# Kernel tuning notes

Hardware: AMD Instinct MI355X
Metric: run time of the kernel (lower is better)

The kernel has to match this reference:

```python
import jax, jax.numpy as jnp
import numpy as np

N_NODES = 50000
N_EDGES = 400000
F_IN = 70
E_DIM = 4
HID = 128
HEADS = 4


def _add_self_loops(src, dst, edge_attr, n):
    # PyG GATConv(add_self_loops=True, fill_value='mean' when edge_dim is set):
    # self-loop edge_attr = per-dst-node mean of incoming edge_attr.
    cnt = jax.ops.segment_sum(jnp.ones((src.shape[0],), edge_attr.dtype), dst, n)
    loop_attr = jax.ops.segment_sum(edge_attr, dst, n) / jnp.clip(cnt, 1.0)[:, None]
    loop = jnp.arange(n, dtype=src.dtype)
    return (jnp.concatenate([src, loop]), jnp.concatenate([dst, loop]),
            jnp.concatenate([edge_attr, loop_attr], axis=0))


def _gat_layer(x, src, dst, e_attr, W, a_src, a_dst, We, a_edge, b, concat):
    # W: [in, H*D]; a_src/a_dst/a_edge: [H, D]; We: [edge_dim, H*D]
    n = x.shape[0]
    H, D = a_src.shape
    xs = (x @ W).reshape(n, H, D)                      # [N,H,D]
    s_src = jnp.einsum('nhd,hd->nh', xs, a_src)        # [N,H]
    s_dst = jnp.einsum('nhd,hd->nh', xs, a_dst)
    ee = (e_attr @ We).reshape(-1, H, D)               # [E,H,D]
    s_edge = jnp.einsum('ehd,hd->eh', ee, a_edge)
    alpha = jax.nn.leaky_relu(s_src[src] + s_dst[dst] + s_edge, 0.2)  # [E,H]
    # segment softmax over edges grouped by destination node
    m = jax.ops.segment_max(alpha, dst, n)
    m = jnp.where(jnp.isfinite(m), m, 0.0)
    ex = jnp.exp(alpha - m[dst])
    denom = jax.ops.segment_sum(ex, dst, n)
    alpha = ex / (denom[dst] + 1e-16)
    msg = xs[src] * alpha[..., None]                   # [E,H,D] -- dominant traffic
    agg = jax.ops.segment_sum(msg, dst, n)             # [N,H,D]
    out = agg.reshape(n, H * D) if concat else agg.mean(axis=1)
    return out + b


def _layer_norm(x, g, b, eps=1e-5):
    mu = x.mean(-1, keepdims=True)
    var = ((x - mu) ** 2).mean(-1, keepdims=True)
    return (x - mu) * jax.lax.rsqrt(var + eps) * g + b


def setup_inputs() -> dict:
    key = jax.random.key(0)
    ks = jax.random.split(key, 24)
    f32 = jnp.float32
    node_features = jax.random.normal(ks[0], (N_NODES, F_IN), f32)
    edge_index = jax.random.randint(ks[1], (2, N_EDGES), 0, N_NODES, jnp.int32)
    edge_attr = jax.random.uniform(ks[2], (N_EDGES, E_DIM), f32)
    s = 0.1
    return {
        'node_features': node_features,
        'edge_index': edge_index,
        'edge_attr': edge_attr,
        'W1': jax.random.normal(ks[3], (F_IN, HEADS * HID), f32) * s,
        'as1': jax.random.normal(ks[4], (HEADS, HID), f32) * s,
        'ad1': jax.random.normal(ks[5], (HEADS, HID), f32) * s,
        'We1': jax.random.normal(ks[6], (E_DIM, HEADS * HID), f32) * s,
        'ae1': jax.random.normal(ks[7], (HEADS, HID), f32) * s,
        'b1': jnp.zeros((HEADS * HID,), f32),
        # GAT layer 2: 512 -> 128, 1 head, mean
        'W2': jax.random.normal(ks[8], (HEADS * HID, HID), f32) * s,
        'as2': jax.random.normal(ks[9], (1, HID), f32) * s,
        'ad2': jax.random.normal(ks[10], (1, HID), f32) * s,
        'We2': jax.random.normal(ks[11], (E_DIM, HID), f32) * s,
        'ae2': jax.random.normal(ks[12], (1, HID), f32) * s,
        'b2': jnp.zeros((HID,), f32),
        'ln_g': jnp.ones((HID,), f32),
        'ln_b': jnp.zeros((HID,), f32),
        'pw': jax.random.normal(ks[13], (HID, 8), f32) * s,
        'pb': jnp.zeros((8,), f32),
        'dw': jax.random.normal(ks[14], (HID, 4), f32) * s,
        'db': jnp.zeros((4,), f32),
    }


def reference(node_features, edge_index, edge_attr, W1, as1, ad1, We1, ae1, b1,
              W2, as2, ad2, We2, ae2, b2, ln_g, ln_b, pw, pb, dw, db):
    n = node_features.shape[0]
    src, dst, ea = _add_self_loops(edge_index[0], edge_index[1], edge_attr, n)
    x = jax.nn.gelu(_gat_layer(node_features, src, dst, ea, W1, as1, ad1, We1, ae1, b1, True), approximate=False)
    x = jax.nn.gelu(_gat_layer(x, src, dst, ea, W2, as2, ad2, We2, ae2, b2, False), approximate=False)
    x = _layer_norm(x, ln_g, ln_b)
    return (x @ pw + pb, x @ dw + db)
```

## Files before the change

kernel.cpp:

```cpp
#include <hip/hip_runtime.h>
#include <hip/hip_bf16.h>
#include <math.h>

#define NN 50000
#define NE 400000
#define FIN 70
#define EDIM 4
#define HIDD 128
#define NHEAD 4
constexpr int ET = NE + NN;
constexpr int KP1 = 96;
constexpr int NFP = 72;
constexpr int SCB = (NN + 255) / 256;

constexpr size_t al4(size_t x){ return (x + 3) & ~size_t(3); }
constexpr size_t CNT_O   = 0;
constexpr size_t ZEND    = al4(CNT_O + NN);
constexpr size_t CSR_O   = ZEND;
constexpr size_t BSUM_O  = al4(CSR_O + NN + 1);
constexpr size_t BOFF_O  = al4(BSUM_O + 256);
constexpr size_t EPK_O   = al4(BOFF_O + 256);
constexpr size_t EXF1_O  = al4(EPK_O + (size_t)ET*4);
constexpr size_t EXF2_O  = al4(EXF1_O + (size_t)ET*4);
constexpr size_t SS1_O   = al4(EXF2_O + ET);
constexpr size_t SD1_O   = al4(SS1_O + (size_t)NN*4);
constexpr size_t SS2_O   = al4(SD1_O + (size_t)NN*4);
constexpr size_t SD2_O   = al4(SS2_O + NN);
constexpr size_t CST_O   = al4(SD2_O + NN);
constexpr size_t W1T_O   = al4(CST_O + 2048);
constexpr size_t W2T_O   = al4(W1T_O + 4*128*KP1/2);
constexpr size_t NFB_O   = al4(W2T_O + 128*512/2);
constexpr size_t AGG_O   = al4(NFB_O + (size_t)NN*NFP/2);
constexpr size_t X1_O    = al4(AGG_O + (size_t)4*NN*KP1/2);
constexpr size_t XS2_O   = al4(X1_O + (size_t)NN*512/2);

constexpr int VS1 = 0;
constexpr int VD1 = 320;
constexpr int VE1 = 640;
constexpr int VE2 = 656;
constexpr int VS2 = 704;
constexpr int VD2 = 1216;

typedef short s8v __attribute__((ext_vector_type(8)));
typedef float f4v __attribute__((ext_vector_type(4)));

__device__ __forceinline__ float gelu_exact(float x){
  return 0.5f * x * (1.f + erff(x * 0.70710678118654752440f));
}
__device__ __forceinline__ unsigned short f2b(float v){
  __hip_bfloat16 b = __float2bfloat16(v);
  return *(unsigned short*)&b;
}
__device__ __forceinline__ float b2f(unsigned u_lo16){
  return __uint_as_float(u_lo16 << 16);
}
__device__ __forceinline__ unsigned pk2(float lo, float hi){
  return (unsigned)f2b(lo) | ((unsigned)f2b(hi) << 16);
}
__device__ __forceinline__ float lrelu(float x){ return x > 0.f ? x : 0.2f * x; }

__global__ void k_deg(const int* __restrict__ ei, int* __restrict__ cnt){
  int e = blockIdx.x * 256 + threadIdx.x;
  if (e >= NE) return;
  atomicAdd(&cnt[ei[NE + e]], 1);
}

__global__ void k_scan1(const int* __restrict__ cnt, int* __restrict__ bsum){
  __shared__ int ws[4];
  int t = threadIdx.x, lane = t & 63, w = t >> 6;
  int i = blockIdx.x * 256 + t;
  int v = (i < NN) ? cnt[i] + 1 : 0;
  for (int o = 32; o; o >>= 1) v += __shfl_down(v, o);
  if (lane == 0) ws[w] = v;
  __syncthreads();
  if (t == 0) bsum[blockIdx.x] = ws[0] + ws[1] + ws[2] + ws[3];
}

__global__ void k_scan2(const int* __restrict__ bsum, int* __restrict__ boff){
  __shared__ int ws[4];
  int t = threadIdx.x, lane = t & 63, w = t >> 6;
  int v = (t < SCB) ? bsum[t] : 0;
  int x = v;
  #pragma unroll
  for (int o = 1; o < 64; o <<= 1){ int u = __shfl_up(x, o); if (lane >= o) x += u; }
  if (lane == 63) ws[w] = x;
  __syncthreads();
  if (w == 0 && lane < 4){
    int y = ws[lane];
    #pragma unroll
    for (int o = 1; o < 4; o <<= 1){ int u = __shfl_up(y, o); if (lane >= o) y += u; }
    ws[lane] = y;
  }
  __syncthreads();
  int incl = x + (w > 0 ? ws[w - 1] : 0);
  if (t < SCB) boff[t] = incl - v;
}

__global__ void k_scan3(const int* __restrict__ cnt, const int* __restrict__ boff,
                        int* __restrict__ csr){
  __shared__ int ws[4];
  int t = threadIdx.x, lane = t & 63, w = t >> 6;
  int i = blockIdx.x * 256 + t;
  int v = (i < NN) ? cnt[i] + 1 : 0;
  int x = v;
  #pragma unroll
  for (int o = 1; o < 64; o <<= 1){ int u = __shfl_up(x, o); if (lane >= o) x += u; }
  if (lane == 63) ws[w] = x;
  __syncthreads();
  if (w == 0 && lane < 4){
    int y = ws[lane];
    #pragma unroll
    for (int o = 1; o < 4; o <<= 1){ int u = __shfl_up(y, o); if (lane >= o) y += u; }
    ws[lane] = y;
  }
  __syncthreads();
  if (i < NN) csr[i + 1] = boff[blockIdx.x] + (w > 0 ? ws[w - 1] : 0) + x;
  if (i == 0) csr[0] = 0;
}

__global__ void k_fill(const int* __restrict__ ei, const float* __restrict__ ea,
                       const int* __restrict__ csr, int* __restrict__ cnt,
                       int4* __restrict__ epk, const float* __restrict__ ss1,
                       const float* __restrict__ sd1, const float* __restrict__ C,
                       float4* __restrict__ exf){
  int e = blockIdx.x * 256 + threadIdx.x;
  if (e >= NE) return;
  int s = ei[e], d = ei[NE + e];
  int r = atomicSub(&cnt[d], 1);
  int p = csr[d] + r - 1;
  float4 a = *(const float4*)&ea[(size_t)e * 4];
  epk[p] = make_int4(s, d, (int)pk2(a.x, a.y), (int)pk2(a.z, a.w));
  float4 ssv = *(const float4*)&ss1[(size_t)s * 4];
  float4 sdv = *(const float4*)&sd1[(size_t)d * 4];
  float e0 = __expf(lrelu(ssv.x + sdv.x + a.x*C[VE1+0] + a.y*C[VE1+4] + a.z*C[VE1+8]  + a.w*C[VE1+12]));
  float e1 = __expf(lrelu(ssv.y + sdv.y + a.x*C[VE1+1] + a.y*C[VE1+5] + a.z*C[VE1+9]  + a.w*C[VE1+13]));
  float e2 = __expf(lrelu(ssv.z + sdv.z + a.x*C[VE1+2] + a.y*C[VE1+6] + a.z*C[VE1+10] + a.w*C[VE1+14]));
  float e3 = __expf(lrelu(ssv.w + sdv.w + a.x*C[VE1+3] + a.y*C[VE1+7] + a.z*C[VE1+11] + a.w*C[VE1+15]));
  exf[p] = make_float4(e0, e1, e2, e3);
}

__global__ void k_loopself(const int* __restrict__ csr, int4* __restrict__ epk,
                           const float* __restrict__ ss1, const float* __restrict__ sd1,
                           const float* __restrict__ C, float4* __restrict__ exf){
  int n = blockIdx.x * 256 + threadIdx.x;
  if (n >= NN) return;
  int a = csr[n], b = csr[n + 1];
  int deg = b - a - 1;
  float s0 = 0.f, s1 = 0.f, s2 = 0.f, s3 = 0.f;
  for (int p = a; p < b - 1; ++p){
    int4 v = epk[p];
    s0 += b2f((unsigned)v.z & 0xffffu); s1 += b2f((unsigned)v.z >> 16);
    s2 += b2f((unsigned)v.w & 0xffffu); s3 += b2f((unsigned)v.w >> 16);
  }
  float inv = 1.f / (float)(deg > 1 ? deg : 1);
  float m0 = s0*inv, m1 = s1*inv, m2 = s2*inv, m3 = s3*inv;
  epk[b - 1] = make_int4(n, n, (int)pk2(m0, m1), (int)pk2(m2, m3));
  float4 ssv = *(const float4*)&ss1[(size_t)n * 4];
  float4 sdv = *(const float4*)&sd1[(size_t)n * 4];
  float e0 = __expf(lrelu(ssv.x + sdv.x + m0*C[VE1+0] + m1*C[VE1+4] + m2*C[VE1+8]  + m3*C[VE1+12]));
  float e1 = __expf(lrelu(ssv.y + sdv.y + m0*C[VE1+1] + m1*C[VE1+5] + m2*C[VE1+9]  + m3*C[VE1+13]));
  float e2 = __expf(lrelu(ssv.z + sdv.z + m0*C[VE1+2] + m1*C[VE1+6] + m2*C[VE1+10] + m3*C[VE1+14]));
  float e3 = __expf(lrelu(ssv.w + sdv.w + m0*C[VE1+3] + m1*C[VE1+7] + m2*C[VE1+11] + m3*C[VE1+15]));
  exf[b - 1] = make_float4(e0, e1, e2, e3);
}

__global__ void k_prep(const float* __restrict__ W1, const float* __restrict__ as1,
                       const float* __restrict__ ad1, const float* __restrict__ We1,
                       const float* __restrict__ ae1, const float* __restrict__ W2,
                       const float* __restrict__ as2, const float* __restrict__ ad2,
                       const float* __restrict__ We2, const float* __restrict__ ae2,
                       float* __restrict__ C){
  int t = threadIdx.x;
  if (t < 280){
    int k = t >> 2, h = t & 3;
    float s = 0.f, d = 0.f;
    for (int dd = 0; dd < 128; ++dd){
      float w = W1[k*512 + h*128 + dd];
      s += w * as1[h*128 + dd];
      d += w * ad1[h*128 + dd];
    }
    C[VS1 + t] = s; C[VD1 + t] = d;
  }
  if (t < 16){
    int k = t >> 2, h = t & 3;
    float s = 0.f;
    for (int dd = 0; dd < 128; ++dd) s += We1[k*512 + h*128 + dd] * ae1[h*128 + dd];
    C[VE1 + t] = s;
  }
  if (t < 4){
    float s = 0.f;
    for (int dd = 0; dd < 128; ++dd) s += We2[t*128 + dd] * ae2[dd];
    C[VE2 + t] = s;
  }
  {
    float s = 0.f, d = 0.f;
    for (int dd = 0; dd < 128; ++dd){
      float w = W2[t*128 + dd];
      s += w * as2[dd];
      d += w * ad2[dd];
    }
    C[VS2 + t] = s; C[VD2 + t] = d;
  }
}

__global__ void k_tw(const float* __restrict__ W1, const float* __restrict__ W2,
                     unsigned short* __restrict__ W1t, unsigned short* __restrict__ W2t){
  int i = blockIdx.x * 256 + threadIdx.x;
  if (i < 4*128*KP1){
    int k = i % KP1, n = (i / KP1) & 127, h = i / (KP1*128);
    float v = (k < FIN) ? W1[k*512 + h*128 + n] : 0.f;
    W1t[i] = f2b(v);
  } else {
    int j = i - 4*128*KP1;
    if (j < 128*512){
      int k = j & 511, n = j >> 9;
      W2t[j] = f2b(W2[k*128 + n]);
    }
  }
}

__global__ __launch_bounds__(256) void k_cnfs1(const float* __restrict__ nf,
    const float* __restrict__ C, unsigned short* __restrict__ nfb,
    float* __restrict__ ss1, float* __restrict__ sd1){
  int lane = threadIdx.x & 63, w = threadIdx.x >> 6;
  int n = blockIdx.x * 4 + w;
  if (n >= NN) return;
  int c0 = lane * 2;
  bool act = lane < 35;
  float v0 = 0.f, v1 = 0.f;
  if (act){
    v0 = nf[(size_t)n * FIN + c0];
    v1 = nf[(size_t)n * FIN + c0 + 1];
  }
  if (lane < 36) *(unsigned*)&nfb[(size_t)n * NFP + c0] = act ? pk2(v0, v1) : 0u;
  float sh[4] = {0,0,0,0}, dh[4] = {0,0,0,0};
  if (act){
    float4 cs0 = *(const float4*)&C[VS1 + c0*4];
    float4 cs1 = *(const float4*)&C[VS1 + (c0+1)*4];
    float4 cd0 = *(const float4*)&C[VD1 + c0*4];
    float4 cd1 = *(const float4*)&C[VD1 + (c0+1)*4];
    sh[0] = v0*cs0.x + v1*cs1.x; sh[1] = v0*cs0.y + v1*cs1.y;
    sh[2] = v0*cs0.z + v1*cs1.z; sh[3] = v0*cs0.w + v1*cs1.w;
    dh[0] = v0*cd0.x + v1*cd1.x; dh[1] = v0*cd0.y + v1*cd1.y;
    dh[2] = v0*cd0.z + v1*cd1.z; dh[3] = v0*cd0.w + v1*cd1.w;
  }
  #pragma unroll
  for (int o = 32; o; o >>= 1){
    #pragma unroll
    for (int h = 0; h < 4; ++h){
      sh[h] += __shfl_xor(sh[h], o);
      dh[h] += __shfl_xor(dh[h], o);
    }
  }
  if (lane == 0){
    *(float4*)&ss1[(size_t)n*4] = make_float4(sh[0], sh[1], sh[2], sh[3]);
    *(float4*)&sd1[(size_t)n*4] = make_float4(dh[0], dh[1], dh[2], dh[3]);
  }
}

__global__ void k_al2(const int4* __restrict__ epk, const float* __restrict__ ss2,
                      const float* __restrict__ sd2, const float* __restrict__ C,
                      float* __restrict__ ex2){
  int p = blockIdx.x * 256 + threadIdx.x;
  if (p >= ET) return;
  int4 pk = epk[p];
  int s = pk.x, d = pk.y;
  float ax = b2f((unsigned)pk.z & 0xffffu), ay = b2f((unsigned)pk.z >> 16);
  float az = b2f((unsigned)pk.w & 0xffffu), aw = b2f((unsigned)pk.w >> 16);
  ex2[p] = __expf(lrelu(ss2[s] + sd2[d] +
             ax*C[VE2] + ay*C[VE2+1] + az*C[VE2+2] + aw*C[VE2+3]));
}

template<int MODE>
__global__ __launch_bounds__(256) void k_mfma(
    const unsigned short* __restrict__ A, int lda, long aSz,
    const unsigned short* __restrict__ Bt, long bSz,
    void* __restrict__ Cout, const float* __restrict__ bias,
    int M, int KP){
  int z = blockIdx.y;
  A  += (size_t)z * aSz;
  Bt += (size_t)z * bSz;
  __shared__ unsigned short sm[10240];
  unsigned short* As = sm;
  unsigned short* Bs = sm + 5120;
  int tid = threadIdx.x, lane = tid & 63, w = tid >> 6;
  int wm = w & 1, wn = w >> 1;
  int row0 = blockIdx.x * 128;
  f4v acc[4][4] = {};
  int r4 = tid >> 2, c4 = tid & 3;
  for (int k0 = 0; k0 < KP; k0 += 32){
    #pragma unroll
    for (int half = 0; half < 2; ++half){
      int r = r4 + half * 64;
      int gr = row0 + r;
      uint4 va = make_uint4(0,0,0,0);
      if (gr < M) va = *(const uint4*)&A[(size_t)gr * lda + k0 + c4*8];
      *(uint4*)&As[r*40 + c4*8] = va;
      uint4 vb = *(const uint4*)&Bt[(size_t)r * lda + k0 + c4*8];
      *(uint4*)&Bs[r*40 + c4*8] = vb;
    }
    __syncthreads();
    s8v af[4], bf[4];
    #pragma unroll
    for (int i = 0; i < 4; ++i){
      af[i] = *(const s8v*)&As[(wm*64 + i*16 + (lane & 15))*40 + (lane >> 4)*8];
      bf[i] = *(const s8v*)&Bs[(wn*64 + i*16 + (lane & 15))*40 + (lane >> 4)*8];
    }
    #pragma unroll
    for (int mi = 0; mi < 4; ++mi)
      #pragma unroll
      for (int ni = 0; ni < 4; ++ni)
        acc[mi][ni] = __builtin_amdgcn_mfma_f32_16x16x32_bf16(af[mi], bf[ni], acc[mi][ni], 0, 0, 0);
    __syncthreads();
  }
  int cq = lane & 15, rq = lane >> 4;
  float bv[4];
  if (MODE == 1){
    #pragma unroll
    for (int ni = 0; ni < 4; ++ni) bv[ni] = bias[z*128 + wn*64 + ni*16 + cq];
  }
  #pragma unroll
  for (int pass = 0; pass < 2; ++pass){
    if (wm == pass){
      #pragma unroll
      for (int mi = 0; mi < 4; ++mi)
        #pragma unroll
        for (int r = 0; r < 4; ++r){
          int lr = mi*16 + rq*4 + r;
          #pragma unroll
          for (int ni = 0; ni < 4; ++ni){
            float v = acc[mi][ni][r];
            if (MODE == 1) v = gelu_exact(v + bv[ni]);
            sm[lr*136 + wn*64 + ni*16 + cq] = f2b(v);
          }
        }
    }
    __syncthreads();
    #pragma unroll
    for (int j = 0; j < 4; ++j){
      int cid = tid + j*256;
      int lr = cid >> 4, ch = cid & 15;
      int grow = row0 + pass*64 + lr;
      if (grow < M){
        uint4 v = *(const uint4*)&sm[lr*136 + ch*8];
        if (MODE == 1)
          *(uint4*)&((unsigned short*)Cout)[(size_t)grow*512 + z*128 + ch*8] = v;
        else
          *(uint4*)&((unsigned short*)Cout)[(size_t)grow*128 + ch*8] = v;
      }
    }
    __syncthreads();
  }
}

__global__ __launch_bounds__(256) void k_aggnf(const int* __restrict__ csr,
    const int4* __restrict__ epk, const float4* __restrict__ exf,
    const unsigned short* __restrict__ nfb, unsigned short* __restrict__ agg){
  int lane = threadIdx.x & 63, w = threadIdx.x >> 6;
  int n = blockIdx.x * 4 + w;
  if (n >= NN) return;
  int off = __builtin_amdgcn_readfirstlane(csr[n]);
  int end = __builtin_amdgcn_readfirstlane(csr[n + 1]);
  int col = lane * 2;
  bool act = lane < 36;
  float d0=0,d1=0,d2=0,d3=0;
  float a00=0,a01=0,a10=0,a11=0,a20=0,a21=0,a30=0,a31=0;
  int p = off;
  for (; p + 2 <= end; p += 2){
    int s0 = epk[p].x, s1 = epk[p+1].x;
    float4 e0 = exf[p], e1 = exf[p+1];
    unsigned u0 = 0, u1 = 0;
    if (act){
      u0 = *(const unsigned*)&nfb[(size_t)s0 * NFP + col];
      u1 = *(const unsigned*)&nfb[(size_t)s1 * NFP + col];
    }
    d0 += e0.x + e1.x; d1 += e0.y + e1.y; d2 += e0.z + e1.z; d3 += e0.w + e1.w;
    float v00 = b2f(u0 & 0xffffu), v01 = b2f(u0 >> 16);
    float v10 = b2f(u1 & 0xffffu), v11 = b2f(u1 >> 16);
    a00 += e0.x*v00 + e1.x*v10; a01 += e0.x*v01 + e1.x*v11;
    a10 += e0.y*v00 + e1.y*v10; a11 += e0.y*v01 + e1.y*v11;
    a20 += e0.z*v00 + e1.z*v10; a21 += e0.z*v01 + e1.z*v11;
    a30 += e0.w*v00 + e1.w*v10; a31 += e0.w*v01 + e1.w*v11;
  }
  if (p < end){
    int s0 = epk[p].x;
    float4 e0 = exf[p];
    unsigned u0 = 0;
    if (act) u0 = *(const unsigned*)&nfb[(size_t)s0 * NFP + col];
    d0 += e0.x; d1 += e0.y; d2 += e0.z; d3 += e0.w;
    float v00 = b2f(u0 & 0xffffu), v01 = b2f(u0 >> 16);
    a00 += e0.x*v00; a01 += e0.x*v01;
    a10 += e0.y*v00; a11 += e0.y*v01;
    a20 += e0.z*v00; a21 += e0.z*v01;
    a30 += e0.w*v00; a31 += e0.w*v01;
  }
  float i0 = 1.f/(d0+1e-16f), i1 = 1.f/(d1+1e-16f);
  float i2 = 1.f/(d2+1e-16f), i3 = 1.f/(d3+1e-16f);
  constexpr size_t HS = (size_t)NN * KP1;
  size_t base = (size_t)n * KP1 + col;
  if (act){
    *(unsigned*)&agg[base]        = pk2(a00*i0, a01*i0);
    *(unsigned*)&agg[base +   HS] = pk2(a10*i1, a11*i1);
    *(unsigned*)&agg[base + 2*HS] = pk2(a20*i2, a21*i2);
    *(unsigned*)&agg[base + 3*HS] = pk2(a30*i3, a31*i3);
  } else if (lane < 48){
    *(unsigned*)&agg[base]        = 0u;
    *(unsigned*)&agg[base +   HS] = 0u;
    *(unsigned*)&agg[base + 2*HS] = 0u;
    *(unsigned*)&agg[base + 3*HS] = 0u;
  }
}

__global__ void k_s2(const unsigned short* __restrict__ x1, const float* __restrict__ C,
                     float* __restrict__ ss2, float* __restrict__ sd2){
  int tid = threadIdx.x, lane = tid & 63;
  int n = blockIdx.x * 4 + (tid >> 6);
  if (n >= NN) return;
  uint4 xv = *(const uint4*)&x1[(size_t)n * 512 + lane * 8];
  float xf[8];
  xf[0] = b2f(xv.x & 0xffffu); xf[1] = b2f(xv.x >> 16);
  xf[2] = b2f(xv.y & 0xffffu); xf[3] = b2f(xv.y >> 16);
  xf[4] = b2f(xv.z & 0xffffu); xf[5] = b2f(xv.z >> 16);
  xf[6] = b2f(xv.w & 0xffffu); xf[7] = b2f(xv.w >> 16);
  float s = 0.f, d = 0.f;
  #pragma unroll
  for (int j = 0; j < 8; ++j){
    s += xf[j] * C[VS2 + lane*8 + j];
    d += xf[j] * C[VD2 + lane*8 + j];
  }
  for (int o = 32; o; o >>= 1){ s += __shfl_down(s, o); d += __shfl_down(d, o); }
  if (lane == 0){ ss2[n] = s; sd2[n] = d; }
}

__global__ __launch_bounds__(256) void k_agg2(
    const int* __restrict__ csr, const int4* __restrict__ epk,
    const float* __restrict__ ex2, const unsigned short* __restrict__ xs2b,
    const float* __restrict__ b2, const float* __restrict__ lng,
    const float* __restrict__ lnb, const float* __restrict__ pw,
    const float* __restrict__ pb, const float* __restrict__ dwm,
    const float* __restrict__ dbv, float* __restrict__ out){
  int lane = threadIdx.x & 63, w = threadIdx.x >> 6;
  int n = blockIdx.x * 4 + w;
  if (n >= NN) return;
  int off = __builtin_amdgcn_readfirstlane(csr[n]);
  int end = __builtin_amdgcn_readfirstlane(csr[n + 1]);
  int c0 = lane * 2;
  float acc0 = 0.f, acc1 = 0.f, den = 0.f;
  int p = off;
  for (; p + 4 <= end; p += 4){
    int s0 = epk[p].x, s1 = epk[p+1].x, s2 = epk[p+2].x, s3 = epk[p+3].x;
    float e0 = ex2[p], e1 = ex2[p+1], e2 = ex2[p+2], e3 = ex2[p+3];
    unsigned u0 = *(const unsigned*)&xs2b[(size_t)s0 * 128 + c0];
    unsigned u1 = *(const unsigned*)&xs2b[(size_t)s1 * 128 + c0];
    unsigned u2 = *(const unsigned*)&xs2b[(size_t)s2 * 128 + c0];
    unsigned u3 = *(const unsigned*)&xs2b[(size_t)s3 * 128 + c0];
    den += (e0 + e1) + (e2 + e3);
    acc0 += e0*b2f(u0 & 0xffffu) + e1*b2f(u1 & 0xffffu)
          + e2*b2f(u2 & 0xffffu) + e3*b2f(u3 & 0xffffu);
    acc1 += e0*b2f(u0 >> 16) + e1*b2f(u1 >> 16)
          + e2*b2f(u2 >> 16) + e3*b2f(u3 >> 16);
  }
  for (; p + 2 <= end; p += 2){
    int s0 = epk[p].x, s1 = epk[p+1].x;
    float e0 = ex2[p], e1 = ex2[p+1];
    unsigned u0 = *(const unsigned*)&xs2b[(size_t)s0 * 128 + c0];
    unsigned u1 = *(const unsigned*)&xs2b[(size_t)s1 * 128 + c0];
    den += e0 + e1;
    acc0 += e0*b2f(u0 & 0xffffu) + e1*b2f(u1 & 0xffffu);
    acc1 += e0*b2f(u0 >> 16) + e1*b2f(u1 >> 16);
  }
  if (p < end){
    int s0 = epk[p].x;
    float e0 = ex2[p];
    unsigned u0 = *(const unsigned*)&xs2b[(size_t)s0 * 128 + c0];
    den += e0;
    acc0 += e0*b2f(u0 & 0xffffu);
    acc1 += e0*b2f(u0 >> 16);
  }
  float invd = 1.f / (den + 1e-16f);
  float g0 = gelu_exact(acc0 * invd + b2[c0]);
  float g1 = gelu_exact(acc1 * invd + b2[c0 + 1]);
  float s = g0 + g1;
  #pragma unroll
  for (int o = 32; o; o >>= 1) s += __shfl_xor(s, o);
  float mu = s * (1.f / 128.f);
  float e0 = g0 - mu, e1 = g1 - mu;
  float q = e0*e0 + e1*e1;
  #pragma unroll
  for (int o = 32; o; o >>= 1) q += __shfl_xor(q, o);
  float rstd = rsqrtf(q * (1.f / 128.f) + 1e-5f);
  float y0 = e0 * rstd * lng[c0] + lnb[c0];
  float y1 = e1 * rstd * lng[c0 + 1] + lnb[c0 + 1];
  float pr[12];
  #pragma unroll
  for (int j = 0; j < 8; ++j) pr[j] = y0 * pw[c0*8 + j] + y1 * pw[(c0+1)*8 + j];
  #pragma unroll
  for (int j = 0; j < 4; ++j) pr[8+j] = y0 * dwm[c0*4 + j] + y1 * dwm[(c0+1)*4 + j];
  #pragma unroll
  for (int o = 32; o; o >>= 1)
    #pragma unroll
    for (int j = 0; j < 12; ++j) pr[j] += __shfl_xor(pr[j], o);
  if (lane == 0){
    #pragma unroll
    for (int j = 0; j < 8; ++j) out[(size_t)n*8 + j] = pr[j] + pb[j];
    #pragma unroll
    for (int j = 0; j < 4; ++j) out[(size_t)NN*8 + (size_t)n*4 + j] = pr[8+j] + dbv[j];
  }
}

extern "C" void kernel_launch(void* const* d_in, const int* in_sizes, int n_in,
                              void* d_out, int out_size, void* d_ws, size_t ws_size,
                              hipStream_t stream){
  const float* nf  = (const float*)d_in[0];
  const int*   ei  = (const int*)  d_in[1];
  const float* ea  = (const float*)d_in[2];
  const float* W1  = (const float*)d_in[3];
  const float* as1 = (const float*)d_in[4];
  const float* ad1 = (const float*)d_in[5];
  const float* We1 = (const float*)d_in[6];
  const float* ae1 = (const float*)d_in[7];
  const float* b1  = (const float*)d_in[8];
  const float* W2  = (const float*)d_in[9];
  const float* as2 = (const float*)d_in[10];
  const float* ad2 = (const float*)d_in[11];
  const float* We2 = (const float*)d_in[12];
  const float* ae2 = (const float*)d_in[13];
  const float* b2  = (const float*)d_in[14];
  const float* lng = (const float*)d_in[15];
  const float* lnb = (const float*)d_in[16];
  const float* pw  = (const float*)d_in[17];
  const float* pb  = (const float*)d_in[18];
  const float* dw  = (const float*)d_in[19];
  const float* db  = (const float*)d_in[20];
  float* out = (float*)d_out;

  float* wf = (float*)d_ws;
  int*      cnt  = (int*)     (wf + CNT_O);
  int*      csr  = (int*)     (wf + CSR_O);
  int*      bsum = (int*)     (wf + BSUM_O);
  int*      boff = (int*)     (wf + BOFF_O);
  int4*     epk  = (int4*)    (wf + EPK_O);
  float4*   exf1 = (float4*)  (wf + EXF1_O);
  float*    ex2  =            (wf + EXF2_O);
  float*    ss1  =            (wf + SS1_O);
  float*    sd1  =            (wf + SD1_O);
  float*    ss2  =            (wf + SS2_O);
  float*    sd2  =            (wf + SD2_O);
  float*    Cc   =            (wf + CST_O);
  unsigned short* W1t = (unsigned short*)(wf + W1T_O);
  unsigned short* W2t = (unsigned short*)(wf + W2T_O);
  unsigned short* nfb = (unsigned short*)(wf + NFB_O);
  unsigned short* agg = (unsigned short*)(wf + AGG_O);
  unsigned short* x1  = (unsigned short*)(wf + X1_O);
  unsigned short* xs2b= (unsigned short*)(wf + XS2_O);

  hipMemsetAsync(cnt, 0, NN * sizeof(int), stream);
  k_prep<<<1, 512, 0, stream>>>(W1, as1, ad1, We1, ae1, W2, as2, ad2, We2, ae2, Cc);
  k_tw<<<(4*128*KP1 + 128*512 + 255) / 256, 256, 0, stream>>>(W1, W2, W1t, W2t);
  k_cnfs1<<<(NN + 3) / 4, 256, 0, stream>>>(nf, Cc, nfb, ss1, sd1);
  k_deg<<<(NE + 255) / 256, 256, 0, stream>>>(ei, cnt);
  k_scan1<<<SCB, 256, 0, stream>>>(cnt, bsum);
  k_scan2<<<1, 256, 0, stream>>>(bsum, boff);
  k_scan3<<<SCB, 256, 0, stream>>>(cnt, boff, csr);
  k_fill<<<(NE + 255) / 256, 256, 0, stream>>>(ei, ea, csr, cnt, epk, ss1, sd1, Cc, exf1);
  k_loopself<<<(NN + 255) / 256, 256, 0, stream>>>(csr, epk, ss1, sd1, Cc, exf1);
  k_aggnf<<<(NN + 3) / 4, 256, 0, stream>>>(csr, epk, exf1, nfb, agg);
  k_mfma<1><<<dim3((NN + 127) / 128, 4), 256, 0, stream>>>(
      agg, KP1, (long)NN * KP1, W1t, (long)128 * KP1, x1, b1, NN, KP1);
  k_s2<<<(NN + 3) / 4, 256, 0, stream>>>(x1, Cc, ss2, sd2);
  k_mfma<2><<<dim3((NN + 127) / 128, 1), 256, 0, stream>>>(
      x1, 512, 0, W2t, 0, xs2b, nullptr, NN, 512);
  k_al2<<<(ET + 255) / 256, 256, 0, stream>>>(epk, ss2, sd2, Cc, ex2);
  k_agg2<<<(NN + 3) / 4, 256, 0, stream>>>(csr, epk, ex2, xs2b,
                                           b2, lng, lnb, pw, pb, dw, db, out);
}
```

Baseline: 387.4 us.

## Use direct-to-LDS swizzled loads in MFMA GEMM, fuse layer-2 score dots, fast GELU

The MFMA GEMM now loads A and B tiles with global_load_lds into an XOR-swizzled, unpadded LDS layout. The MFMA operands are swapped so each lane can write four bf16 results straight to global memory, which drops the LDS-staged epilogue and its barriers. The separate k_s2 kernel is removed: the per-node attention dot products for layer 2 are computed inside the layer-2 GEMM from the A tiles already sitting in LDS. Exact erf-based GELU is replaced with an Abramowitz-Stegun polynomial approximation, which adds a small numerical error in exchange for cheaper math.

```diff
diff --git a/kernel.cpp b/kernel.cpp
--- a/kernel.cpp
+++ b/kernel.cpp
@@ -44,9 +44,6 @@
 typedef short s8v __attribute__((ext_vector_type(8)));
 typedef float f4v __attribute__((ext_vector_type(4)));
 
-__device__ __forceinline__ float gelu_exact(float x){
-  return 0.5f * x * (1.f + erff(x * 0.70710678118654752440f));
-}
 __device__ __forceinline__ unsigned short f2b(float v){
   __hip_bfloat16 b = __float2bfloat16(v);
   return *(unsigned short*)&b;
@@ -58,6 +55,23 @@
   return (unsigned)f2b(lo) | ((unsigned)f2b(hi) << 16);
 }
 __device__ __forceinline__ float lrelu(float x){ return x > 0.f ? x : 0.2f * x; }
+
+__device__ __forceinline__ float gelu_fast(float x){
+  float z = x * 0.70710678118654752440f;
+  float a = fabsf(z);
+  float t = 1.f / (1.f + 0.3275911f * a);
+  float p = ((((1.061405429f*t - 1.453152027f)*t + 1.421413741f)*t
+              - 0.284496736f)*t + 0.254829592f)*t;
+  float erfv = 1.f - p * __expf(-a * a);
+  erfv = copysignf(erfv, z);
+  return 0.5f * x * (1.f + erfv);
+}
+
+__device__ __forceinline__ void gl16(const unsigned short* g, unsigned short* l){
+  __builtin_amdgcn_global_load_lds(
+      (const __attribute__((address_space(1))) unsigned int*)g,
+      (__attribute__((address_space(3))) unsigned int*)l, 16, 0, 0);
+}
 
 __global__ void k_deg(const int* __restrict__ ei, int* __restrict__ cnt){
   int e = blockIdx.x * 256 + threadIdx.x;
@@ -275,81 +289,91 @@
 __global__ __launch_bounds__(256) void k_mfma(
     const unsigned short* __restrict__ A, int lda, long aSz,
     const unsigned short* __restrict__ Bt, long bSz,
-    void* __restrict__ Cout, const float* __restrict__ bias,
+    unsigned short* __restrict__ Cout, const float* __restrict__ bias,
+    const float* __restrict__ Cv, float* __restrict__ ss2, float* __restrict__ sd2,
     int M, int KP){
   int z = blockIdx.y;
   A  += (size_t)z * aSz;
   Bt += (size_t)z * bSz;
-  __shared__ unsigned short sm[10240];
-  unsigned short* As = sm;
-  unsigned short* Bs = sm + 5120;
+  __shared__ unsigned short As[128 * 32];
+  __shared__ unsigned short Bs[128 * 32];
   int tid = threadIdx.x, lane = tid & 63, w = tid >> 6;
   int wm = w & 1, wn = w >> 1;
   int row0 = blockIdx.x * 128;
   f4v acc[4][4] = {};
-  int r4 = tid >> 2, c4 = tid & 3;
+  int rl = lane >> 2, cslot = lane & 3;
+  int m15 = lane & 15, j = lane >> 4;
+  float s2a = 0.f, s2d = 0.f;
+  int sr = tid >> 1, shf = tid & 1;
+  int ssw = (sr ^ (sr >> 2)) & 3;
   for (int k0 = 0; k0 < KP; k0 += 32){
     #pragma unroll
     for (int half = 0; half < 2; ++half){
-      int r = r4 + half * 64;
-      int gr = row0 + r;
-      uint4 va = make_uint4(0,0,0,0);
-      if (gr < M) va = *(const uint4*)&A[(size_t)gr * lda + k0 + c4*8];
-      *(uint4*)&As[r*40 + c4*8] = va;
-      uint4 vb = *(const uint4*)&Bt[(size_t)r * lda + k0 + c4*8];
-      *(uint4*)&Bs[r*40 + c4*8] = vb;
+      int rb = w * 16 + half * 64;
+      int r = rb + rl;
+      int cs = cslot ^ ((r ^ (r >> 2)) & 3);
+      int gr = row0 + r; if (gr >= M) gr = M - 1;
+      gl16(A + (size_t)gr * lda + k0 + cs * 8, &As[rb * 32]);
+      gl16(Bt + (size_t)r * lda + k0 + cs * 8, &Bs[rb * 32]);
     }
     __syncthreads();
     s8v af[4], bf[4];
     #pragma unroll
-    for (int i = 0; i < 4; ++i){
-      af[i] = *(const s8v*)&As[(wm*64 + i*16 + (lane & 15))*40 + (lane >> 4)*8];
-      bf[i] = *(const s8v*)&Bs[(wn*64 + i*16 + (lane & 15))*40 + (lane >> 4)*8];
+    for (int t = 0; t < 4; ++t){
+      int ra = wm*64 + t*16 + m15;
+      af[t] = *(const s8v*)&As[ra*32 + ((j ^ ((ra ^ (ra >> 2)) & 3)) * 8)];
+      int rb2 = wn*64 + t*16 + m15;
+      bf[t] = *(const s8v*)&Bs[rb2*32 + ((j ^ ((rb2 ^ (rb2 >> 2)) & 3)) * 8)];
+    }
+    if (MODE == 2){
+      #pragma unroll
+      for (int cc = 0; cc < 2; ++cc){
+        int c = shf * 2 + cc;
+        int kb = k0 + ((c ^ ssw) * 8);
+        s8v xv = *(const s8v*)&As[sr*32 + c*8];
+        #pragma unroll
+        for (int t2 = 0; t2 < 8; ++t2){
+          float xf = b2f((unsigned short)xv[t2]);
+          s2a += xf * Cv[VS2 + kb + t2];
+          s2d += xf * Cv[VD2 + kb + t2];
+        }
+      }
     }
     #pragma unroll
     for (int mi = 0; mi < 4; ++mi)
       #pragma unroll
       for (int ni = 0; ni < 4; ++ni)
-        acc[mi][ni] = __builtin_amdgcn_mfma_f32_16x16x32_bf16(af[mi], bf[ni], acc[mi][ni], 0, 0, 0);
+        acc[mi][ni] = __builtin_amdgcn_mfma_f32_16x16x32_bf16(bf[ni], af[mi], acc[mi][ni], 0, 0, 0);
     __syncthreads();
   }
   int cq = lane & 15, rq = lane >> 4;
-  float bv[4];
-  if (MODE == 1){
-    #pragma unroll
-    for (int ni = 0; ni < 4; ++ni) bv[ni] = bias[z*128 + wn*64 + ni*16 + cq];
-  }
-  #pragma unroll
-  for (int pass = 0; pass < 2; ++pass){
-    if (wm == pass){
+  #pragma unroll
+  for (int mi = 0; mi < 4; ++mi){
+    int grow = row0 + wm*64 + mi*16 + cq;
+    if (grow < M){
       #pragma unroll
-      for (int mi = 0; mi < 4; ++mi)
-        #pragma unroll
-        for (int r = 0; r < 4; ++r){
-          int lr = mi*16 + rq*4 + r;
-          #pragma unroll
-          for (int ni = 0; ni < 4; ++ni){
-            float v = acc[mi][ni][r];
-            if (MODE == 1) v = gelu_exact(v + bv[ni]);
-            sm[lr*136 + wn*64 + ni*16 + cq] = f2b(v);
-          }
+      for (int ni = 0; ni < 4; ++ni){
+        int gc = wn*64 + ni*16 + rq*4;
+        float v0 = acc[mi][ni][0], v1 = acc[mi][ni][1];
+        float v2 = acc[mi][ni][2], v3 = acc[mi][ni][3];
+        if (MODE == 1){
+          float4 bv = *(const float4*)&bias[z*128 + gc];
+          v0 = gelu_fast(v0 + bv.x); v1 = gelu_fast(v1 + bv.y);
+          v2 = gelu_fast(v2 + bv.z); v3 = gelu_fast(v3 + bv.w);
+          *(uint2*)&Cout[(size_t)grow*512 + z*128 + gc] = make_uint2(pk2(v0,v1), pk2(v2,v3));
+        } else {
+          *(uint2*)&Cout[(size_t)grow*128 + gc] = make_uint2(pk2(v0,v1), pk2(v2,v3));
         }
-    }
-    __syncthreads();
-    #pragma unroll
-    for (int j = 0; j < 4; ++j){
-      int cid = tid + j*256;
-      int lr = cid >> 4, ch = cid & 15;
-      int grow = row0 + pass*64 + lr;
-      if (grow < M){
-        uint4 v = *(const uint4*)&sm[lr*136 + ch*8];
-        if (MODE == 1)
-          *(uint4*)&((unsigned short*)Cout)[(size_t)grow*512 + z*128 + ch*8] = v;
-        else
-          *(uint4*)&((unsigned short*)Cout)[(size_t)grow*128 + ch*8] = v;
       }
     }
-    __syncthreads();
+  }
+  if (MODE == 2){
+    float oa = s2a + __shfl_xor(s2a, 1);
+    float od = s2d + __shfl_xor(s2d, 1);
+    if (shf == 0){
+      int grow = row0 + sr;
+      if (grow < M){ ss2[grow] = oa; sd2[grow] = od; }
+    }
   }
 }
 
@@ -409,27 +433,6 @@
     *(unsigned*)&agg[base + 2*HS] = 0u;
     *(unsigned*)&agg[base + 3*HS] = 0u;
   }
-}
-
-__global__ void k_s2(const unsigned short* __restrict__ x1, const float* __restrict__ C,
-                     float* __restrict__ ss2, float* __restrict__ sd2){
-  int tid = threadIdx.x, lane = tid & 63;
-  int n = blockIdx.x * 4 + (tid >> 6);
-  if (n >= NN) return;
-  uint4 xv = *(const uint4*)&x1[(size_t)n * 512 + lane * 8];
-  float xf[8];
-  xf[0] = b2f(xv.x & 0xffffu); xf[1] = b2f(xv.x >> 16);
-  xf[2] = b2f(xv.y & 0xffffu); xf[3] = b2f(xv.y >> 16);
-  xf[4] = b2f(xv.z & 0xffffu); xf[5] = b2f(xv.z >> 16);
-  xf[6] = b2f(xv.w & 0xffffu); xf[7] = b2f(xv.w >> 16);
-  float s = 0.f, d = 0.f;
-  #pragma unroll
-  for (int j = 0; j < 8; ++j){
-    s += xf[j] * C[VS2 + lane*8 + j];
-    d += xf[j] * C[VD2 + lane*8 + j];
-  }
-  for (int o = 32; o; o >>= 1){ s += __shfl_down(s, o); d += __shfl_down(d, o); }
-  if (lane == 0){ ss2[n] = s; sd2[n] = d; }
 }
 
 __global__ __launch_bounds__(256) void k_agg2(
@@ -478,8 +481,8 @@
     acc1 += e0*b2f(u0 >> 16);
   }
   float invd = 1.f / (den + 1e-16f);
-  float g0 = gelu_exact(acc0 * invd + b2[c0]);
-  float g1 = gelu_exact(acc1 * invd + b2[c0 + 1]);
+  float g0 = gelu_fast(acc0 * invd + b2[c0]);
+  float g1 = gelu_fast(acc1 * invd + b2[c0 + 1]);
   float s = g0 + g1;
   #pragma unroll
   for (int o = 32; o; o >>= 1) s += __shfl_xor(s, o);
@@ -493,18 +496,18 @@
   float y1 = e1 * rstd * lng[c0 + 1] + lnb[c0 + 1];
   float pr[12];
   #pragma unroll
-  for (int j = 0; j < 8; ++j) pr[j] = y0 * pw[c0*8 + j] + y1 * pw[(c0+1)*8 + j];
-  #pragma unroll
-  for (int j = 0; j < 4; ++j) pr[8+j] = y0 * dwm[c0*4 + j] + y1 * dwm[(c0+1)*4 + j];
+  for (int jj = 0; jj < 8; ++jj) pr[jj] = y0 * pw[c0*8 + jj] + y1 * pw[(c0+1)*8 + jj];
+  #pragma unroll
+  for (int jj = 0; jj < 4; ++jj) pr[8+jj] = y0 * dwm[c0*4 + jj] + y1 * dwm[(c0+1)*4 + jj];
   #pragma unroll
   for (int o = 32; o; o >>= 1)
     #pragma unroll
-    for (int j = 0; j < 12; ++j) pr[j] += __shfl_xor(pr[j], o);
+    for (int jj = 0; jj < 12; ++jj) pr[jj] += __shfl_xor(pr[jj], o);
   if (lane == 0){
     #pragma unroll
-    for (int j = 0; j < 8; ++j) out[(size_t)n*8 + j] = pr[j] + pb[j];
-    #pragma unroll
-    for (int j = 0; j < 4; ++j) out[(size_t)NN*8 + (size_t)n*4 + j] = pr[8+j] + dbv[j];
+    for (int jj = 0; jj < 8; ++jj) out[(size_t)n*8 + jj] = pr[jj] + pb[jj];
+    #pragma unroll
+    for (int jj = 0; jj < 4; ++jj) out[(size_t)NN*8 + (size_t)n*4 + jj] = pr[8+jj] + dbv[jj];
   }
 }
 
@@ -566,10 +569,10 @@
   k_loopself<<<(NN + 255) / 256, 256, 0, stream>>>(csr, epk, ss1, sd1, Cc, exf1);
   k_aggnf<<<(NN + 3) / 4, 256, 0, stream>>>(csr, epk, exf1, nfb, agg);
   k_mfma<1><<<dim3((NN + 127) / 128, 4), 256, 0, stream>>>(
-      agg, KP1, (long)NN * KP1, W1t, (long)128 * KP1, x1, b1, NN, KP1);
-  k_s2<<<(NN + 3) / 4, 256, 0, stream>>>(x1, Cc, ss2, sd2);
+      agg, KP1, (long)NN * KP1, W1t, (long)128 * KP1, x1, b1,
+      nullptr, nullptr, nullptr, NN, KP1);
   k_mfma<2><<<dim3((NN + 127) / 128, 1), 256, 0, stream>>>(
-      x1, 512, 0, W2t, 0, xs2b, nullptr, NN, 512);
+      x1, 512, 0, W2t, 0, xs2b, nullptr, Cc, ss2, sd2, NN, 512);
   k_al2<<<(ET + 255) / 256, 256, 0, stream>>>(epk, ss2, sd2, Cc, ex2);
   k_agg2<<<(NN + 3) / 4, 256, 0, stream>>>(csr, epk, ex2, xs2b,
                                            b2, lng, lnb, pw, pb, dw, db, out);
```

Measured after the change: 372.9 us. -3.7%, faster.
